# Performance work log

Hardware: AMD Instinct MI355X
Metric: run time of the kernel (lower is better)

## Reference

```python
import jax, jax.numpy as jnp
import numpy as np

UNITS = 128
INPUT_SIZE = 64
BATCH = 2048
SDE_UNFOLDS = 6
ODE_UNFOLDS = 6


def setup_inputs() -> dict:
    key = jax.random.key(0)
    ks = jax.random.split(key, 16)
    U, I, B = UNITS, INPUT_SIZE, BATCH
    inp = {
        "inputs": jax.random.normal(ks[0], (B, I), dtype=jnp.float32),
        "states": jax.random.normal(ks[1], (B, U), dtype=jnp.float32),
        "input_weights": jnp.ones((I,), dtype=jnp.float32),
        "input_biases": jnp.zeros((I,), dtype=jnp.float32),
        "sensory_mu": jax.random.uniform(ks[2], (I, U), minval=0.3, maxval=0.8, dtype=jnp.float32),
        "sensory_sigma": jax.random.uniform(ks[3], (I, U), minval=3.0, maxval=8.0, dtype=jnp.float32),
        "sensory_W": jax.random.uniform(ks[4], (I, U), minval=0.01, maxval=1.0, dtype=jnp.float32),
        "sensory_erev": (2.0 * jax.random.randint(ks[5], (I, U), 0, 2).astype(jnp.float32) - 1.0),
        "mu": jax.random.uniform(ks[6], (U, U), minval=0.3, maxval=0.8, dtype=jnp.float32),
        "sigma": jax.random.uniform(ks[7], (U, U), minval=3.0, maxval=8.0, dtype=jnp.float32),
        "W": jax.random.uniform(ks[8], (U, U), minval=0.01, maxval=1.0, dtype=jnp.float32),
        "erev": (2.0 * jax.random.randint(ks[9], (U, U), 0, 2).astype(jnp.float32) - 1.0),
        "vleak": jax.random.uniform(ks[10], (U,), minval=-0.2, maxval=0.2, dtype=jnp.float32),
        "gleak": jnp.ones((U,), dtype=jnp.float32),   # gleak_init_min == gleak_init_max == 1
        "cm_t": jnp.full((U,), 0.5, dtype=jnp.float32),  # cm_init_min == cm_init_max == 0.5
    }
    return inp


def _syn_sigmoid(v, mu, sigma):
    # v: [B, D]; mu, sigma: [D, U] -> [B, D, U]
    return jax.nn.sigmoid(sigma * (v[:, :, None] - mu))


def reference(inputs, states, input_weights, input_biases,
              sensory_mu, sensory_sigma, sensory_W, sensory_erev,
              mu, sigma, W, erev, vleak, gleak, cm_t):
    # affine input mapping
    x = inputs * input_weights + input_biases  # [B, I]

    # sensory synaptic activation (constant across unfolds, compute once)
    sens_act = sensory_W * _syn_sigmoid(x, sensory_mu, sensory_sigma)  # [B, I, U]
    w_num_s = jnp.sum(sens_act * sensory_erev, axis=1)  # [B, U]
    w_den_s = jnp.sum(sens_act, axis=1)                 # [B, U]

    def drift(v):
        # inner LTC fused ODE solver (6 unfolds)
        for _ in range(ODE_UNFOLDS):
            w_act = W * _syn_sigmoid(v, mu, sigma)      # [B, U, U]
            w_num = jnp.sum(w_act * erev, axis=1) + w_num_s
            w_den = jnp.sum(w_act, axis=1) + w_den_s
            v = (cm_t * v + gleak * vleak + w_num) / (cm_t + gleak + w_den)
        return v

    # Euler-Maruyama outer loop; diffusion term is unimplemented (None) in the
    # source, treated as zero, so states += drift * time_step (time_step = 1)
    s = states
    for _ in range(SDE_UNFOLDS):
        s = s + drift(s)
    return s
```

## Files before the change

kernel.cpp:

```cpp
#include <hip/hip_runtime.h>


#define LOG2E 1.4426950408889634f

constexpr int U   = 128;
constexpr int I   = 64;
constexpr int B   = 2048;
constexpr int M   = 4;
constexpr int S   = 4;
constexpr int BLK = 512;
constexpr int RPT = U / S;
constexpr int SDE = 6, ODE = 6;

#if __has_builtin(__builtin_amdgcn_exp2f)
#define EXP2(x) __builtin_amdgcn_exp2f(x)
#else
#define EXP2(x) exp2f(x)
#endif
#if __has_builtin(__builtin_amdgcn_rcpf)
#define RCP(x) __builtin_amdgcn_rcpf(x)
#else
#define RCP(x) (1.0f / (x))
#endif

#define SIGACC(P, V, PN, PD)                                   \
  {                                                            \
    float t_ = fmaf((P).x, (V), (P).y);                        \
    float e_ = EXP2(t_);                                       \
    float r_ = RCP(1.0f + e_);                                 \
    (PN) = fmaf((P).z, r_, (PN));                              \
    (PD) = fmaf((P).w, r_, (PD));                              \
  }

__global__ __launch_bounds__(256) void pack_params(
    const float* __restrict__ mu, const float* __restrict__ sigma,
    const float* __restrict__ W, const float* __restrict__ erev,
    const float* __restrict__ smu, const float* __restrict__ ssig,
    const float* __restrict__ sW, const float* __restrict__ serev,
    float4* __restrict__ pp, float4* __restrict__ ps)
{
  int idx = blockIdx.x * 256 + threadIdx.x;
  if (idx < U * U) {
    float sg = sigma[idx];
    float w  = W[idx];
    pp[idx] = make_float4(-LOG2E * sg, LOG2E * sg * mu[idx], w * erev[idx], w);
  } else if (idx < U * U + I * U) {
    int k = idx - U * U;
    float sg = ssig[k];
    float w  = sW[k];
    ps[k] = make_float4(-LOG2E * sg, LOG2E * sg * smu[k], w * serev[k], w);
  }
}

__global__ __launch_bounds__(BLK)
__attribute__((amdgpu_waves_per_eu(2, 2)))
void ltc_kernel(
    const float4* __restrict__ pp, const float4* __restrict__ ps,
    const float* __restrict__ inputs, const float* __restrict__ states,
    const float* __restrict__ iw, const float* __restrict__ ibias,
    const float* __restrict__ vleak, const float* __restrict__ gleak,
    const float* __restrict__ cmt, float* __restrict__ out)
{
  __shared__ __align__(16) float4 v4[2][M][U / 4];
  __shared__ __align__(16) float x_lds[M][I];

  const int tid = threadIdx.x;
  const int jlo = tid & 15;
  const int s   = (tid >> 4) & 3;
  const int j   = ((tid >> 6) << 4) | jlo;
  const int b0  = blockIdx.x * M;

  const float cm = cmt[j];
  const float gl = gleak[j];
  const float gv = gl * vleak[j];
  const float cg = cm + gl;

  float4 P[RPT];
#pragma unroll
  for (int k = 0; k < RPT; ++k) P[k] = pp[(s * RPT + k) * U + j];

  if (tid < M * I) {
    const int m = tid >> 6, i = tid & (I - 1);
    x_lds[m][i] = inputs[(b0 + m) * I + i] * iw[i] + ibias[i];
  }
  __syncthreads();

  float wns[M], wds[M];
  {
    float pn[M], pd[M];
#pragma unroll
    for (int m = 0; m < M; ++m) { pn[m] = 0.f; pd[m] = 0.f; }
#pragma unroll
    for (int q = 0; q < 4; ++q) {
      const int i = s * 16 + q * 4;
      const float4 p0 = ps[(i + 0) * U + j];
      const float4 p1 = ps[(i + 1) * U + j];
      const float4 p2 = ps[(i + 2) * U + j];
      const float4 p3 = ps[(i + 3) * U + j];
#pragma unroll
      for (int m = 0; m < M; ++m) {
        const float4 xv = *reinterpret_cast<const float4*>(&x_lds[m][i]);
        SIGACC(p0, xv.x, pn[m], pd[m]);
        SIGACC(p1, xv.y, pn[m], pd[m]);
        SIGACC(p2, xv.z, pn[m], pd[m]);
        SIGACC(p3, xv.w, pn[m], pd[m]);
      }
    }
#pragma unroll
    for (int m = 0; m < M; ++m) {
      float n = pn[m], d = pd[m];
      n += __shfl_xor(n, 16); n += __shfl_xor(n, 32);
      d += __shfl_xor(d, 16); d += __shfl_xor(d, 32);
      wns[m] = n; wds[m] = d;
    }
  }

#pragma unroll
  for (int k = 0; k < RPT; ++k)
    asm volatile("" : "+v"(P[k].x), "+v"(P[k].y), "+v"(P[k].z), "+v"(P[k].w));

  float sv[M];
#pragma unroll
  for (int m = 0; m < M; ++m) sv[m] = states[(b0 + m) * U + j];

  int buf = 0;
  float vj[M];
  for (int sde = 0; sde < SDE; ++sde) {
#pragma unroll
    for (int m = 0; m < M; ++m) vj[m] = sv[m];
    buf ^= 1;
    if (s == 0) {
#pragma unroll
      for (int m = 0; m < M; ++m)
        reinterpret_cast<float*>(&v4[buf][m][0])[j] = sv[m];
    }
    __syncthreads();

    for (int ode = 0; ode < ODE; ++ode) {
      float pn[M], pd[M];
#pragma unroll
      for (int m = 0; m < M; ++m) { pn[m] = 0.f; pd[m] = 0.f; }
#pragma unroll
      for (int q = 0; q < 8; ++q) {
#pragma unroll
        for (int m = 0; m < M; ++m) {
          const float4 vv = v4[buf][m][s * 8 + q];
          SIGACC(P[q * 4 + 0], vv.x, pn[m], pd[m]);
          SIGACC(P[q * 4 + 1], vv.y, pn[m], pd[m]);
          SIGACC(P[q * 4 + 2], vv.z, pn[m], pd[m]);
          SIGACC(P[q * 4 + 3], vv.w, pn[m], pd[m]);
        }
      }
#pragma unroll
      for (int m = 0; m < M; ++m) {
        float n = pn[m], d = pd[m];
        n += __shfl_xor(n, 16); n += __shfl_xor(n, 32);
        d += __shfl_xor(d, 16); d += __shfl_xor(d, 32);
        n += wns[m]; d += wds[m];
        const float den = cg + d;
        float r = RCP(den);
        r = r * (2.0f - den * r);
        vj[m] = (fmaf(cm, vj[m], gv) + n) * r;
      }
      buf ^= 1;
      if (s == 0) {
#pragma unroll
        for (int m = 0; m < M; ++m)
          reinterpret_cast<float*>(&v4[buf][m][0])[j] = vj[m];
      }
      __syncthreads();
    }
#pragma unroll
    for (int m = 0; m < M; ++m) sv[m] += vj[m];
  }

  if (s == 0) {
#pragma unroll
    for (int m = 0; m < M; ++m) out[(b0 + m) * U + j] = sv[m];
  }
}

extern "C" void kernel_launch(void* const* d_in, const int* in_sizes, int n_in,
                              void* d_out, int out_size, void* d_ws, size_t ws_size,
                              hipStream_t stream) {
  const float* inputs = (const float*)d_in[0];
  const float* states = (const float*)d_in[1];
  const float* iw     = (const float*)d_in[2];
  const float* ibias  = (const float*)d_in[3];
  const float* smu    = (const float*)d_in[4];
  const float* ssig   = (const float*)d_in[5];
  const float* sW     = (const float*)d_in[6];
  const float* serev  = (const float*)d_in[7];
  const float* mu     = (const float*)d_in[8];
  const float* sigma  = (const float*)d_in[9];
  const float* W      = (const float*)d_in[10];
  const float* erev   = (const float*)d_in[11];
  const float* vleak  = (const float*)d_in[12];
  const float* gleak  = (const float*)d_in[13];
  const float* cmt    = (const float*)d_in[14];
  float* out = (float*)d_out;

  float4* pp = (float4*)d_ws;
  float4* ps = pp + U * U;

  const int packN = U * U + I * U;
  pack_params<<<(packN + 255) / 256, 256, 0, stream>>>(
      mu, sigma, W, erev, smu, ssig, sW, serev, pp, ps);
  ltc_kernel<<<B / M, BLK, 0, stream>>>(
      pp, ps, inputs, states, iw, ibias, vleak, gleak, cmt, out);
}
```

Baseline: 415.6 us.

## Stream synapse params from global/L2 each ODE step and double batch rows per block

Drops the register-resident parameter tile of 32 float4 per thread. Each ODE step now reloads the packed synapse parameters from global memory (served from cache), and each block handles 8 batch rows instead of 4, so every parameter load is amortized over more rows. The LDS read pattern is interleaved by s, and the launch bounds change from a forced waves-per-EU setting to a min-blocks hint. This frees registers and halves the number of blocks, but adds global-load traffic and latency inside the hot loop.

```diff
diff --git a/kernel.cpp b/kernel.cpp
--- a/kernel.cpp
+++ b/kernel.cpp
@@ -6,10 +6,9 @@
 constexpr int U   = 128;
 constexpr int I   = 64;
 constexpr int B   = 2048;
-constexpr int M   = 4;
+constexpr int M   = 8;
 constexpr int S   = 4;
 constexpr int BLK = 512;
-constexpr int RPT = U / S;
 constexpr int SDE = 6, ODE = 6;
 
 #if __has_builtin(__builtin_amdgcn_exp2f)
@@ -52,9 +51,7 @@
   }
 }
 
-__global__ __launch_bounds__(BLK)
-__attribute__((amdgpu_waves_per_eu(2, 2)))
-void ltc_kernel(
+__global__ __launch_bounds__(BLK, 2) void ltc_kernel(
     const float4* __restrict__ pp, const float4* __restrict__ ps,
     const float* __restrict__ inputs, const float* __restrict__ states,
     const float* __restrict__ iw, const float* __restrict__ ibias,
@@ -75,11 +72,7 @@
   const float gv = gl * vleak[j];
   const float cg = cm + gl;
 
-  float4 P[RPT];
-#pragma unroll
-  for (int k = 0; k < RPT; ++k) P[k] = pp[(s * RPT + k) * U + j];
-
-  if (tid < M * I) {
+  {
     const int m = tid >> 6, i = tid & (I - 1);
     x_lds[m][i] = inputs[(b0 + m) * I + i] * iw[i] + ibias[i];
   }
@@ -91,15 +84,15 @@
 #pragma unroll
     for (int m = 0; m < M; ++m) { pn[m] = 0.f; pd[m] = 0.f; }
 #pragma unroll
-    for (int q = 0; q < 4; ++q) {
-      const int i = s * 16 + q * 4;
-      const float4 p0 = ps[(i + 0) * U + j];
-      const float4 p1 = ps[(i + 1) * U + j];
-      const float4 p2 = ps[(i + 2) * U + j];
-      const float4 p3 = ps[(i + 3) * U + j];
+    for (int q = 0; q < I / 16; ++q) {
+      const int i0 = q * 16 + s * 4;
+      const float4 p0 = ps[(i0 + 0) * U + j];
+      const float4 p1 = ps[(i0 + 1) * U + j];
+      const float4 p2 = ps[(i0 + 2) * U + j];
+      const float4 p3 = ps[(i0 + 3) * U + j];
 #pragma unroll
       for (int m = 0; m < M; ++m) {
-        const float4 xv = *reinterpret_cast<const float4*>(&x_lds[m][i]);
+        const float4 xv = *reinterpret_cast<const float4*>(&x_lds[m][i0]);
         SIGACC(p0, xv.x, pn[m], pd[m]);
         SIGACC(p1, xv.y, pn[m], pd[m]);
         SIGACC(p2, xv.z, pn[m], pd[m]);
@@ -115,10 +108,6 @@
     }
   }
 
-#pragma unroll
-  for (int k = 0; k < RPT; ++k)
-    asm volatile("" : "+v"(P[k].x), "+v"(P[k].y), "+v"(P[k].z), "+v"(P[k].w));
-
   float sv[M];
 #pragma unroll
   for (int m = 0; m < M; ++m) sv[m] = states[(b0 + m) * U + j];
@@ -141,14 +130,19 @@
 #pragma unroll
       for (int m = 0; m < M; ++m) { pn[m] = 0.f; pd[m] = 0.f; }
 #pragma unroll
-      for (int q = 0; q < 8; ++q) {
+      for (int q = 0; q < U / 16; ++q) {
+        const int i0 = q * 16 + s * 4;
+        const float4 p0 = pp[(i0 + 0) * U + j];
+        const float4 p1 = pp[(i0 + 1) * U + j];
+        const float4 p2 = pp[(i0 + 2) * U + j];
+        const float4 p3 = pp[(i0 + 3) * U + j];
 #pragma unroll
         for (int m = 0; m < M; ++m) {
-          const float4 vv = v4[buf][m][s * 8 + q];
-          SIGACC(P[q * 4 + 0], vv.x, pn[m], pd[m]);
-          SIGACC(P[q * 4 + 1], vv.y, pn[m], pd[m]);
-          SIGACC(P[q * 4 + 2], vv.z, pn[m], pd[m]);
-          SIGACC(P[q * 4 + 3], vv.w, pn[m], pd[m]);
+          const float4 vv = v4[buf][m][q * 4 + s];
+          SIGACC(p0, vv.x, pn[m], pd[m]);
+          SIGACC(p1, vv.y, pn[m], pd[m]);
+          SIGACC(p2, vv.z, pn[m], pd[m]);
+          SIGACC(p3, vv.w, pn[m], pd[m]);
         }
       }
 #pragma unroll
```

New measurement: 543.2 us. +30.7%, slower.
